# Kernel optimization log

Measured on AMD Instinct MI355X. Metric: run time of the kernel, lower is better.

Reference implementation:

```python
import jax, jax.numpy as jnp
import numpy as np

EPS = 1e-5  # torch BatchNorm1d default eps
N, E, F, H, P = 50000, 640000, 128, 128, 64


def batch_norm(h):
    # track_running_stats=False, affine=False -> per-batch mean / biased var
    mu = jnp.mean(h, axis=0)
    var = jnp.mean((h - mu) ** 2, axis=0)
    return (h - mu) * jax.lax.rsqrt(var + EPS)


def gcn_conv(x, src, dst, W, b, n_nodes):
    # GCNConv: D^{-1/2} (A + I) D^{-1/2} X W + b
    h = x @ W
    loop = jnp.arange(n_nodes)
    s = jnp.concatenate([src, loop])
    d = jnp.concatenate([dst, loop])
    deg = jax.ops.segment_sum(jnp.ones(s.shape[0], h.dtype), d, num_segments=n_nodes)
    inv_sqrt = jax.lax.rsqrt(jnp.maximum(deg, 1.0))  # deg >= 1 due to self loops
    msg = h[s] * (inv_sqrt[s] * inv_sqrt[d])[:, None]  # [E+N, H]
    return jax.ops.segment_sum(msg, d, num_segments=n_nodes) + b


def setup_inputs() -> dict:
    key = jax.random.key(0)
    ks = jax.random.split(key, 12)
    s = 0.05
    return {
        "x": jax.random.normal(ks[0], (N, F), jnp.float32),
        "core_values": jax.random.uniform(ks[1], (N,), jnp.float32),
        "W0": jax.random.normal(ks[2], (F, H), jnp.float32) * s,
        "b0": jnp.zeros((H,), jnp.float32),
        "W1": jax.random.normal(ks[3], (H, H), jnp.float32) * s,
        "b1": jnp.zeros((H,), jnp.float32),
        "lin1_W": jax.random.normal(ks[4], (3 * H, H), jnp.float32) * s,
        "lin1_b": jnp.zeros((H,), jnp.float32),
        "lin2_W": jax.random.normal(ks[5], (H, 1), jnp.float32) * s,
        "lin2_b": jnp.zeros((1,), jnp.float32),
        "edge_index": jax.random.randint(ks[6], (2, E), 0, N, jnp.int64 if jax.config.read("jax_enable_x64") else jnp.int32),
        "part_id": jax.random.randint(ks[7], (N,), 0, P, jnp.int32),
        "curr_node_id": 123,
        "num_partitions": P,
    }


def reference(x, core_values, W0, b0, W1, b1, lin1_W, lin1_b, lin2_W, lin2_b,
              edge_index, part_id, curr_node_id, num_partitions):
    n_nodes = x.shape[0]
    src, dst = edge_index[0], edge_index[1]

    # GNN stack: conv -> batchnorm -> relu (num_layers = 2)
    for W, b in ((W0, b0), (W1, b1)):
        x = jax.nn.relu(batch_norm(gcn_conv(x, src, dst, W, b, n_nodes)))

    # getPartitonEmbedding_usingCoreValue as fused segment reductions
    cv = core_values[:, None]
    core = jax.ops.segment_sum(x * cv, part_id, num_segments=num_partitions)
    non_core = jax.ops.segment_sum(x * (1.0 - cv), part_id, num_segments=num_partitions)
    partition_embedding = jnp.concatenate([core, non_core], axis=1)  # [P, 2H]

    x_curr = jnp.broadcast_to(x[curr_node_id][None, :], (num_partitions, x.shape[1]))
    z = jnp.concatenate([x_curr, partition_embedding], axis=1)  # [P, 3H]
    z = jax.nn.relu(z @ lin1_W + lin1_b)
    return z @ lin2_W + lin2_b  # [P, 1]
```

## Files before the change

kernel.cpp:

```cpp
#include <hip/hip_runtime.h>
#include <math.h>

#define EPSV 1e-5f
#define PSORT_NB 256
#define SCAN_NB 256

typedef __attribute__((ext_vector_type(8))) short bf16x8;
typedef __attribute__((ext_vector_type(4))) float f32x4;

__device__ __forceinline__ uint f2b(float f) {
  uint u = __builtin_bit_cast(uint, f);
  return (u + 0x7FFFu + ((u >> 16) & 1u)) >> 16;
}
__device__ __forceinline__ float blo(uint v) { return __builtin_bit_cast(float, v << 16); }
__device__ __forceinline__ float bhi(uint v) { return __builtin_bit_cast(float, v & 0xFFFF0000u); }
__device__ __forceinline__ float b2f(ushort u) { return __builtin_bit_cast(float, ((uint)u) << 16); }

__global__ __launch_bounds__(256) void k_pre1(int* __restrict__ hist, int nbZero,
                                              const int* __restrict__ part,
                                              int* __restrict__ blockHist,
                                              const float* __restrict__ W0,
                                              const float* __restrict__ W1,
                                              ushort* __restrict__ WT0,
                                              ushort* __restrict__ WT1, int n) {
  const int b = blockIdx.x, tid = threadIdx.x;
  if (b < nbZero) {
    int i = b * 256 + tid;
    if (i < n) hist[i] = 0;
  } else if (b < nbZero + PSORT_NB) {
    __shared__ int lh[64];
    int pb = b - nbZero;
    if (tid < 64) lh[tid] = 0;
    __syncthreads();
    int chunk = (n + PSORT_NB - 1) / PSORT_NB;
    int beg = pb * chunk, end = min(n, beg + chunk);
    for (int i = beg + tid; i < end; i += 256) atomicAdd(&lh[part[i]], 1);
    __syncthreads();
    if (tid < 64) blockHist[pb * 64 + tid] = lh[tid];
  } else {
    int idx = (b - nbZero - PSORT_NB) * 256 + tid;
    const float* W = (idx < 16384) ? W0 : W1;
    ushort* WT = (idx < 16384) ? WT0 : WT1;
    int j = idx & 16383;
    int c = j >> 7, k = j & 127;
    WT[j] = (ushort)f2b(W[k * 128 + c]);
  }
}

__global__ __launch_bounds__(256) void k_pre2(const int* __restrict__ dst,
                                              int* __restrict__ hist,
                                              int* __restrict__ rank, int e, int eb,
                                              const int* __restrict__ blockHist,
                                              int* __restrict__ base,
                                              int* __restrict__ ptot) {
  const int b = blockIdx.x, tid = threadIdx.x;
  if (b < eb) {
    int i = b * 256 + tid;
    if (i < e) rank[i] = atomicAdd(&hist[dst[i]], 1);
  } else {
    __shared__ int wtot[4];
    const int p = b - eb;
    const int lane = tid & 63, w = tid >> 6;
    int v = blockHist[tid * 64 + p];
    int x = v;
    #pragma unroll
    for (int off = 1; off < 64; off <<= 1) {
      int y = __shfl_up(x, off);
      if (lane >= off) x += y;
    }
    if (lane == 63) wtot[w] = x;
    __syncthreads();
    int woff = 0;
    if (w > 0) woff = wtot[0];
    if (w > 1) woff += wtot[1];
    if (w > 2) woff += wtot[2];
    base[tid * 64 + p] = woff + x - v;
    if (tid == 255) ptot[p] = woff + x;
  }
}

__global__ __launch_bounds__(256) void k_pre3(const int* __restrict__ hist,
                                              int* __restrict__ row_start,
                                              float* __restrict__ invs,
                                              int* __restrict__ bsum, int n,
                                              const int* __restrict__ ptot,
                                              int* __restrict__ pexcl,
                                              int* __restrict__ pstart) {
  const int b = blockIdx.x, tid = threadIdx.x;
  if (b < SCAN_NB) {
    __shared__ int wtot[4];
    __shared__ int tot;
    const int lane = tid & 63, w = tid >> 6;
    const int chunk = (n + SCAN_NB - 1) / SCAN_NB;
    const int beg = b * chunk, end = min(n, beg + chunk);
    int running = 0;
    for (int t0 = beg; t0 < end; t0 += 256) {
      int i = t0 + tid;
      int v = (i < end) ? hist[i] : 0;
      int x = v;
      #pragma unroll
      for (int off = 1; off < 64; off <<= 1) {
        int y = __shfl_up(x, off);
        if (lane >= off) x += y;
      }
      if (lane == 63) wtot[w] = x;
      __syncthreads();
      if (tid == 0) {
        int a0 = wtot[0], a1 = wtot[1], a2 = wtot[2], a3 = wtot[3];
        wtot[0] = 0; wtot[1] = a0; wtot[2] = a0 + a1; wtot[3] = a0 + a1 + a2;
        tot = a0 + a1 + a2 + a3;
      }
      __syncthreads();
      if (i < end) {
        row_start[i] = running + wtot[w] + x - v;
        invs[i] = rsqrtf((float)(v + 1));
      }
      running += tot;
      __syncthreads();
    }
    if (tid == 0) bsum[b] = running;
  } else if (tid < 64) {
    int v = ptot[tid];
    int x = v;
    #pragma unroll
    for (int off = 1; off < 64; off <<= 1) {
      int y = __shfl_up(x, off);
      if (tid >= off) x += y;
    }
    int excl = x - v;
    pexcl[tid] = excl;
    pstart[tid] = excl;
    if (tid == 63) pstart[64] = x;
  }
}

__global__ __launch_bounds__(256) void k_pre4(const int* __restrict__ bsum,
                                              int* __restrict__ boff,
                                              int* __restrict__ row_fin, int n,
                                              const int* __restrict__ part,
                                              const int* __restrict__ base,
                                              const int* __restrict__ pexcl,
                                              int* __restrict__ perm) {
  const int b = blockIdx.x, tid = threadIdx.x;
  if (b == 0) {
    if (tid < 64) {
      int v0 = bsum[tid * 4], v1 = bsum[tid * 4 + 1], v2 = bsum[tid * 4 + 2], v3 = bsum[tid * 4 + 3];
      int s = v0 + v1 + v2 + v3;
      int x = s;
      #pragma unroll
      for (int off = 1; off < 64; off <<= 1) {
        int y = __shfl_up(x, off);
        if (tid >= off) x += y;
      }
      int run = x - s;
      boff[tid * 4] = run; run += v0;
      boff[tid * 4 + 1] = run; run += v1;
      boff[tid * 4 + 2] = run; run += v2;
      boff[tid * 4 + 3] = run;
      if (tid == 63) row_fin[n] = x;
    }
  } else {
    __shared__ int cur[64];
    const int pb = b - 1;
    if (tid < 64) cur[tid] = base[pb * 64 + tid] + pexcl[tid];
    __syncthreads();
    int chunk = (n + PSORT_NB - 1) / PSORT_NB;
    int beg = pb * chunk, end = min(n, beg + chunk);
    for (int i = beg + tid; i < end; i += 256) {
      int pos = atomicAdd(&cur[part[i]], 1);
      perm[pos] = i;
    }
  }
}

template <bool BN>
__device__ __forceinline__ void gemm_body(ushort* As, ushort* Bs, float* muL, float* sclL,
                                          const void* __restrict__ inp,
                                          const ushort* __restrict__ WT,
                                          const float* __restrict__ invs,
                                          const float* __restrict__ stats_red,
                                          ushort* __restrict__ outb, int n, int bb) {
  const int tid = threadIdx.x;
  const int l = tid & 63, w = tid >> 6;
  const int br0 = bb * 128;

  if (BN) {
    if (tid < 128) {
      float s = stats_red[tid], q = stats_red[128 + tid];
      float m = s * (1.0f / 50000.0f);
      muL[tid] = m;
      sclL[tid] = rsqrtf(q * (1.0f / 50000.0f) - m * m + EPSV);
    }
    __syncthreads();
  }

  #pragma unroll
  for (int i = 0; i < 8; ++i) {
    int flat = i * 2048 + tid * 8;
    int c = flat >> 7;
    uint4 v = *(const uint4*)&WT[flat];
    *(uint4*)&Bs[flat ^ ((c & 7) << 3)] = v;
  }
  #pragma unroll
  for (int i = 0; i < 8; ++i) {
    int flat = i * 2048 + tid * 8;
    int row = flat >> 7, k0 = flat & 127;
    int grow = br0 + row;
    uint4 u;
    if (grow < n) {
      if (BN) {
        const ushort* inb = (const ushort*)inp;
        uint4 raw = *(const uint4*)&inb[(size_t)grow * 128 + k0];
        float f[8] = {blo(raw.x), bhi(raw.x), blo(raw.y), bhi(raw.y),
                      blo(raw.z), bhi(raw.z), blo(raw.w), bhi(raw.w)};
        #pragma unroll
        for (int j = 0; j < 8; ++j) {
          float v = (f[j] - muL[k0 + j]) * sclL[k0 + j];
          f[j] = v > 0.f ? v : 0.f;
        }
        u.x = f2b(f[0]) | (f2b(f[1]) << 16);
        u.y = f2b(f[2]) | (f2b(f[3]) << 16);
        u.z = f2b(f[4]) | (f2b(f[5]) << 16);
        u.w = f2b(f[6]) | (f2b(f[7]) << 16);
      } else {
        const float* inf = (const float*)inp;
        float4 v0 = *(const float4*)&inf[(size_t)grow * 128 + k0];
        float4 v1 = *(const float4*)&inf[(size_t)grow * 128 + k0 + 4];
        u.x = f2b(v0.x) | (f2b(v0.y) << 16);
        u.y = f2b(v0.z) | (f2b(v0.w) << 16);
        u.z = f2b(v1.x) | (f2b(v1.y) << 16);
        u.w = f2b(v1.z) | (f2b(v1.w) << 16);
      }
    } else {
      u.x = u.y = u.z = u.w = 0u;
    }
    *(uint4*)&As[flat ^ ((row & 7) << 3)] = u;
  }
  __syncthreads();

  const int wr = w >> 1, wc = w & 1;
  const int lr = l & 15, lk = (l >> 4) * 8;
  f32x4 acc[4][4];
  #pragma unroll
  for (int m = 0; m < 4; ++m)
    #pragma unroll
    for (int nn = 0; nn < 4; ++nn) acc[m][nn] = (f32x4){0.f, 0.f, 0.f, 0.f};

  #pragma unroll
  for (int ks = 0; ks < 4; ++ks) {
    bf16x8 af[4], bfr[4];
    #pragma unroll
    for (int m = 0; m < 4; ++m) {
      int row = wr * 64 + m * 16 + lr;
      af[m] = *(const bf16x8*)&As[(row * 128 + ks * 32 + lk) ^ ((row & 7) << 3)];
    }
    #pragma unroll
    for (int nn = 0; nn < 4; ++nn) {
      int c = wc * 64 + nn * 16 + lr;
      bfr[nn] = *(const bf16x8*)&Bs[(c * 128 + ks * 32 + lk) ^ ((c & 7) << 3)];
    }
    #pragma unroll
    for (int m = 0; m < 4; ++m)
      #pragma unroll
      for (int nn = 0; nn < 4; ++nn)
        acc[m][nn] = __builtin_amdgcn_mfma_f32_16x16x32_bf16(af[m], bfr[nn], acc[m][nn], 0, 0, 0);
  }

  #pragma unroll
  for (int m = 0; m < 4; ++m) {
    #pragma unroll
    for (int r = 0; r < 4; ++r) {
      int row = br0 + wr * 64 + m * 16 + (l >> 4) * 4 + r;
      if (row >= n) continue;
      float iv = invs[row];
      #pragma unroll
      for (int nn = 0; nn < 4; ++nn) {
        int col = wc * 64 + nn * 16 + lr;
        outb[(size_t)row * 128 + col] = (ushort)f2b(acc[m][nn][r] * iv);
      }
    }
  }
}

__global__ __launch_bounds__(256) void k_mega1(const float* __restrict__ x,
                                               const ushort* __restrict__ WT0,
                                               const float* __restrict__ invs,
                                               ushort* __restrict__ hsb, int n, int gb,
                                               const int* __restrict__ row_start,
                                               const int* __restrict__ boff,
                                               int* __restrict__ row_fin,
                                               const int* __restrict__ src,
                                               const int* __restrict__ dst,
                                               const int* __restrict__ rank,
                                               int* __restrict__ csr, int e) {
  __shared__ ushort As[16384];
  __shared__ ushort Bs[16384];
  const int b = blockIdx.x, tid = threadIdx.x;
  if (b < gb) {
    gemm_body<false>(As, Bs, nullptr, nullptr, x, WT0, invs, nullptr, hsb, n, b);
  } else if (b < gb + SCAN_NB) {
    const int sb = b - gb;
    const int chunk = (n + SCAN_NB - 1) / SCAN_NB;
    const int beg = sb * chunk, end = min(n, beg + chunk);
    const int off = boff[sb];
    for (int i = beg + tid; i < end; i += 256) row_fin[i] = row_start[i] + off;
  } else {
    const int chunkS = (n + SCAN_NB - 1) / SCAN_NB;
    int i = (b - gb - SCAN_NB) * 256 + tid;
    if (i < e) {
      int d = dst[i];
      csr[row_start[d] + boff[d / chunkS] + rank[i]] = src[i];
    }
  }
}

template <bool BN>
__global__ __launch_bounds__(256) void k_gemm(const void* __restrict__ inp,
                                              const ushort* __restrict__ WT,
                                              const float* __restrict__ invs,
                                              const float* __restrict__ stats_red,
                                              ushort* __restrict__ outb, int n) {
  __shared__ ushort As[16384];
  __shared__ ushort Bs[16384];
  __shared__ float muL[128], sclL[128];
  gemm_body<BN>(As, Bs, muL, sclL, inp, WT, invs, stats_red, outb, n, blockIdx.x);
}

__global__ __launch_bounds__(256) void k_gather(const ushort* __restrict__ hsb,
                                                const int* __restrict__ row_fin,
                                                const int* __restrict__ csr,
                                                const float* __restrict__ invs,
                                                const float* __restrict__ bias,
                                                ushort* __restrict__ outb,
                                                float* __restrict__ statsP, int n) {
  const int tid = threadIdx.x;
  const int lane = tid & 63, w = tid >> 6;
  const int c0 = lane * 2;
  const ushort* hc = hsb + c0;
  float s0 = 0.f, s1 = 0.f, q0 = 0.f, q1 = 0.f;
  const float bv0 = bias[c0], bv1 = bias[c0 + 1];
  const int stride = gridDim.x * 4;
  for (int node = blockIdx.x * 4 + w; node < n; node += stride) {
    uint vs = *(const uint*)&hc[(size_t)node * 128];
    float accx = blo(vs), accy = bhi(vs);
    int beg = row_fin[node], end = row_fin[node + 1];
    int deg = end - beg;
    int base = 0;
    while (base < deg) {
      int cnt = min(deg - base, 64);
      int sidx = 0;
      if (lane < cnt) sidx = csr[beg + base + lane];
      int j = 0;
      for (; j + 7 < cnt; j += 8) {
        int sA = __shfl(sidx, j + 0), sB = __shfl(sidx, j + 1);
        int sC = __shfl(sidx, j + 2), sD = __shfl(sidx, j + 3);
        int sE = __shfl(sidx, j + 4), sF = __shfl(sidx, j + 5);
        int sG = __shfl(sidx, j + 6), sH = __shfl(sidx, j + 7);
        uint vA = *(const uint*)&hc[(size_t)sA * 128];
        uint vB = *(const uint*)&hc[(size_t)sB * 128];
        uint vC = *(const uint*)&hc[(size_t)sC * 128];
        uint vD = *(const uint*)&hc[(size_t)sD * 128];
        uint vE = *(const uint*)&hc[(size_t)sE * 128];
        uint vF = *(const uint*)&hc[(size_t)sF * 128];
        uint vG = *(const uint*)&hc[(size_t)sG * 128];
        uint vH = *(const uint*)&hc[(size_t)sH * 128];
        accx += ((blo(vA) + blo(vB)) + (blo(vC) + blo(vD))) +
                ((blo(vE) + blo(vF)) + (blo(vG) + blo(vH)));
        accy += ((bhi(vA) + bhi(vB)) + (bhi(vC) + bhi(vD))) +
                ((bhi(vE) + bhi(vF)) + (bhi(vG) + bhi(vH)));
      }
      for (; j + 3 < cnt; j += 4) {
        int sA = __shfl(sidx, j + 0), sB = __shfl(sidx, j + 1);
        int sC = __shfl(sidx, j + 2), sD = __shfl(sidx, j + 3);
        uint vA = *(const uint*)&hc[(size_t)sA * 128];
        uint vB = *(const uint*)&hc[(size_t)sB * 128];
        uint vC = *(const uint*)&hc[(size_t)sC * 128];
        uint vD = *(const uint*)&hc[(size_t)sD * 128];
        accx += (blo(vA) + blo(vB)) + (blo(vC) + blo(vD));
        accy += (bhi(vA) + bhi(vB)) + (bhi(vC) + bhi(vD));
      }
      for (; j < cnt; ++j) {
        int sA = __shfl(sidx, j);
        uint vA = *(const uint*)&hc[(size_t)sA * 128];
        accx += blo(vA);
        accy += bhi(vA);
      }
      base += cnt;
    }
    float iv = invs[node];
    float o0 = accx * iv + bv0, o1 = accy * iv + bv1;
    *(uint*)&outb[(size_t)node * 128 + c0] = f2b(o0) | (f2b(o1) << 16);
    s0 += o0; s1 += o1; q0 += o0 * o0; q1 += o1 * o1;
  }
  __shared__ float redS[4][128], redQ[4][128];
  redS[w][c0] = s0; redS[w][c0 + 1] = s1;
  redQ[w][c0] = q0; redQ[w][c0 + 1] = q1;
  __syncthreads();
  if (tid < 128) {
    float s = redS[0][tid] + redS[1][tid] + redS[2][tid] + redS[3][tid];
    statsP[blockIdx.x * 256 + tid] = s;
  } else {
    int t = tid - 128;
    float q = redQ[0][t] + redQ[1][t] + redQ[2][t] + redQ[3][t];
    statsP[blockIdx.x * 256 + tid] = q;
  }
}

__global__ __launch_bounds__(1024) void k_finstats(const float* __restrict__ statsP,
                                                   float* __restrict__ stats_red,
                                                   int nb) {
  int t = threadIdx.x;
  int c = blockIdx.x * 16 + (t & 15);
  int b0 = t >> 4;
  int per = nb >> 6;
  float s = 0.f;
  for (int j = 0; j < per; ++j) s += statsP[(b0 * per + j) * 256 + c];
  __shared__ float red[1024];
  red[t] = s;
  __syncthreads();
  for (int st = 512; st >= 16; st >>= 1) {
    if (t < st) red[t] += red[t + st];
    __syncthreads();
  }
  if (t < 16) stats_red[blockIdx.x * 16 + t] = red[t];
}

__global__ __launch_bounds__(512) void k_pool2(const ushort* __restrict__ hb,
                                               const float* __restrict__ stats_red,
                                               const float* __restrict__ cv,
                                               const int* __restrict__ perm,
                                               const int* __restrict__ pstart,
                                               float* __restrict__ poolP, int n) {
  const int tid = threadIdx.x;
  const int lane = tid & 63, w = tid >> 6;
  const int p = blockIdx.x >> 2, s = blockIdx.x & 3;
  const int g = s * 8 + w;
  const int c0 = lane * 2;

  float s0 = stats_red[c0], s1 = stats_red[c0 + 1];
  float qq0 = stats_red[128 + c0], qq1 = stats_red[128 + c0 + 1];
  float mu0 = s0 * (1.0f / 50000.0f), mu1 = s1 * (1.0f / 50000.0f);
  float scl0 = rsqrtf(qq0 * (1.0f / 50000.0f) - mu0 * mu0 + EPSV);
  float scl1 = rsqrtf(qq1 * (1.0f / 50000.0f) - mu1 * mu1 + EPSV);

  const int beg = pstart[p], end = pstart[p + 1];
  float cc0 = 0.f, cc1 = 0.f, cn0 = 0.f, cn1 = 0.f;

  int j = beg + g;
  for (; j + 32 < end; j += 64) {
    int rA = perm[j], rB = perm[j + 32];
    uint vA = *(const uint*)&hb[(size_t)rA * 128 + c0];
    uint vB = *(const uint*)&hb[(size_t)rB * 128 + c0];
    float cvA = cv[rA], cvB = cv[rB];
    float xA0 = (blo(vA) - mu0) * scl0; xA0 = xA0 > 0.f ? xA0 : 0.f;
    float xA1 = (bhi(vA) - mu1) * scl1; xA1 = xA1 > 0.f ? xA1 : 0.f;
    float xB0 = (blo(vB) - mu0) * scl0; xB0 = xB0 > 0.f ? xB0 : 0.f;
    float xB1 = (bhi(vB) - mu1) * scl1; xB1 = xB1 > 0.f ? xB1 : 0.f;
    cc0 += xA0 * cvA + xB0 * cvB;
    cc1 += xA1 * cvA + xB1 * cvB;
    cn0 += xA0 * (1.f - cvA) + xB0 * (1.f - cvB);
    cn1 += xA1 * (1.f - cvA) + xB1 * (1.f - cvB);
  }
  if (j < end) {
    int rA = perm[j];
    uint vA = *(const uint*)&hb[(size_t)rA * 128 + c0];
    float cvA = cv[rA];
    float xA0 = (blo(vA) - mu0) * scl0; xA0 = xA0 > 0.f ? xA0 : 0.f;
    float xA1 = (bhi(vA) - mu1) * scl1; xA1 = xA1 > 0.f ? xA1 : 0.f;
    cc0 += xA0 * cvA;
    cc1 += xA1 * cvA;
    cn0 += xA0 * (1.f - cvA);
    cn1 += xA1 * (1.f - cvA);
  }

  __shared__ float redC[8][128], redN[8][128];
  redC[w][c0] = cc0; redC[w][c0 + 1] = cc1;
  redN[w][c0] = cn0; redN[w][c0 + 1] = cn1;
  __syncthreads();
  if (tid < 128) {
    float a = 0.f;
    #pragma unroll
    for (int ww = 0; ww < 8; ++ww) a += redC[ww][tid];
    poolP[blockIdx.x * 256 + tid] = a;
  } else if (tid < 256) {
    int t = tid - 128;
    float a = 0.f;
    #pragma unroll
    for (int ww = 0; ww < 8; ++ww) a += redN[ww][t];
    poolP[blockIdx.x * 256 + tid] = a;
  }
}

__global__ __launch_bounds__(128) void k_mlp(const ushort* __restrict__ hb,
                                             const float* __restrict__ stats_red,
                                             const float* __restrict__ poolP,
                                             const float* __restrict__ l1W,
                                             const float* __restrict__ l1b,
                                             const float* __restrict__ l2W,
                                             const float* __restrict__ l2b,
                                             const int* __restrict__ curr_ptr,
                                             float* __restrict__ out, int n) {
  const int p = blockIdx.x;
  const int t = threadIdx.x;
  __shared__ float z[384];
  int curr = *curr_ptr;
  float s = stats_red[t], q = stats_red[128 + t];
  float mu = s / (float)n;
  float scl = rsqrtf(q / (float)n - mu * mu + EPSV);
  float v = b2f(hb[(size_t)curr * 128 + t]);
  v = (v - mu) * scl;
  z[t] = v > 0.f ? v : 0.f;
  float ccore = 0.f, cnon = 0.f;
  #pragma unroll
  for (int sb = 0; sb < 4; ++sb) {
    ccore += poolP[(p * 4 + sb) * 256 + t];
    cnon  += poolP[(p * 4 + sb) * 256 + 128 + t];
  }
  z[128 + t] = ccore;
  z[256 + t] = cnon;
  __syncthreads();
  float a = l1b[t];
  for (int k = 0; k < 384; ++k) a += z[k] * l1W[k * 128 + t];
  a = a > 0.f ? a : 0.f;
  float pr = a * l2W[t];
  #pragma unroll
  for (int off = 32; off; off >>= 1) pr += __shfl_down(pr, off);
  __shared__ float rr[2];
  if ((t & 63) == 0) rr[t >> 6] = pr;
  __syncthreads();
  if (t == 0) out[p] = rr[0] + rr[1] + l2b[0];
}

extern "C" void kernel_launch(void* const* d_in, const int* in_sizes, int n_in,
                              void* d_out, int out_size, void* d_ws, size_t ws_size,
                              hipStream_t stream) {
  const float* x    = (const float*)d_in[0];
  const float* cv   = (const float*)d_in[1];
  const float* W0   = (const float*)d_in[2];
  const float* b0   = (const float*)d_in[3];
  const float* W1   = (const float*)d_in[4];
  const float* b1   = (const float*)d_in[5];
  const float* l1W  = (const float*)d_in[6];
  const float* l1b  = (const float*)d_in[7];
  const float* l2W  = (const float*)d_in[8];
  const float* l2b  = (const float*)d_in[9];
  const int*   ei   = (const int*)d_in[10];
  const int*   part = (const int*)d_in[11];
  const int*   curr = (const int*)d_in[12];

  const int N = in_sizes[1];
  const int E = in_sizes[10] / 2;
  const int* src = ei;
  const int* dst = ei + E;

  const int GATHER_BLOCKS = 2048;

  char* w = (char*)d_ws;
  size_t off = 0;
  auto alloc = [&](size_t bytes) -> void* {
    void* p = (void*)(w + off);
    off = (off + bytes + 255) & ~(size_t)255;
    return p;
  };
  int*   hist      = (int*)alloc((size_t)N * 4);
  int*   row_start = (int*)alloc((size_t)(N + 1) * 4);
  int*   row_fin   = (int*)alloc((size_t)(N + 1) * 4);
  int*   csr       = (int*)alloc((size_t)E * 4);
  int*   rank      = (int*)alloc((size_t)E * 4);
  float* invs      = (float*)alloc((size_t)N * 4);
  int*   bsum      = (int*)alloc((size_t)SCAN_NB * 4);
  int*   boff      = (int*)alloc((size_t)SCAN_NB * 4);
  int*   blockHist = (int*)alloc((size_t)PSORT_NB * 64 * 4);
  int*   pbase     = (int*)alloc((size_t)PSORT_NB * 64 * 4);
  int*   ptot      = (int*)alloc(64 * 4);
  int*   pexcl     = (int*)alloc(64 * 4);
  int*   pstart    = (int*)alloc(65 * 4);
  int*   perm      = (int*)alloc((size_t)N * 4);
  float* stats_red0 = (float*)alloc(256 * 4);
  float* stats_red1 = (float*)alloc(256 * 4);
  float* statsP    = (float*)alloc((size_t)GATHER_BLOCKS * 256 * 4);
  float* poolP     = (float*)alloc((size_t)256 * 256 * 4);
  ushort* WT0      = (ushort*)alloc((size_t)16384 * 2);
  ushort* WT1      = (ushort*)alloc((size_t)16384 * 2);
  ushort* hsb      = (ushort*)alloc((size_t)N * 128 * 2);
  ushort* hb       = (ushort*)alloc((size_t)N * 128 * 2);
  (void)ws_size;

  const int eb = (E + 255) / 256;
  const int nbZero = (N + 255) / 256;
  const int gb = (N + 127) / 128;

  k_pre1<<<nbZero + PSORT_NB + 128, 256, 0, stream>>>(hist, nbZero, part, blockHist,
                                                      W0, W1, WT0, WT1, N);
  k_pre2<<<eb + 64, 256, 0, stream>>>(dst, hist, rank, E, eb, blockHist, pbase, ptot);
  k_pre3<<<SCAN_NB + 1, 256, 0, stream>>>(hist, row_start, invs, bsum, N, ptot, pexcl, pstart);
  k_pre4<<<1 + PSORT_NB, 256, 0, stream>>>(bsum, boff, row_fin, N, part, pbase, pexcl, perm);
  k_mega1<<<gb + SCAN_NB + eb, 256, 0, stream>>>(x, WT0, invs, hsb, N, gb,
                                                 row_start, boff, row_fin,
                                                 src, dst, rank, csr, E);
  k_gather<<<GATHER_BLOCKS, 256, 0, stream>>>(hsb, row_fin, csr, invs, b0, hb, statsP, N);
  k_finstats<<<16, 1024, 0, stream>>>(statsP, stats_red0, GATHER_BLOCKS);
  k_gemm<true><<<gb, 256, 0, stream>>>(hb, WT1, invs, stats_red0, hsb, N);
  k_gather<<<GATHER_BLOCKS, 256, 0, stream>>>(hsb, row_fin, csr, invs, b1, hb, statsP, N);
  k_finstats<<<16, 1024, 0, stream>>>(statsP, stats_red1, GATHER_BLOCKS);
  k_pool2<<<256, 512, 0, stream>>>(hb, stats_red1, cv, perm, pstart, poolP, N);
  k_mlp<<<64, 128, 0, stream>>>(hb, stats_red1, poolP, l1W, l1b, l2W, l2b, curr, (float*)d_out, N);
}
```

Baseline: 176.5 us.

## Move first GEMM earlier by deferring degree scaling into gather

The first-layer GEMM no longer depends on the degree normalization, so it is launched together with the edge-rank atomics and partition scan in one kernel, right after the first preprocessing kernel. The source-side inverse-sqrt-degree scaling for layer one moves into the gather, which now loads invs per neighbor and shuffles it alongside the indices. The CSR fill becomes its own kernel. This overlaps the GEMM with the atomic histogram work. In exchange the first gather does extra per-edge loads and multiplies, and the 4-wide unrolled remainder loop is removed.

```diff
diff --git a/kernel.cpp b/kernel.cpp
--- a/kernel.cpp
+++ b/kernel.cpp
@@ -47,133 +47,7 @@
   }
 }
 
-__global__ __launch_bounds__(256) void k_pre2(const int* __restrict__ dst,
-                                              int* __restrict__ hist,
-                                              int* __restrict__ rank, int e, int eb,
-                                              const int* __restrict__ blockHist,
-                                              int* __restrict__ base,
-                                              int* __restrict__ ptot) {
-  const int b = blockIdx.x, tid = threadIdx.x;
-  if (b < eb) {
-    int i = b * 256 + tid;
-    if (i < e) rank[i] = atomicAdd(&hist[dst[i]], 1);
-  } else {
-    __shared__ int wtot[4];
-    const int p = b - eb;
-    const int lane = tid & 63, w = tid >> 6;
-    int v = blockHist[tid * 64 + p];
-    int x = v;
-    #pragma unroll
-    for (int off = 1; off < 64; off <<= 1) {
-      int y = __shfl_up(x, off);
-      if (lane >= off) x += y;
-    }
-    if (lane == 63) wtot[w] = x;
-    __syncthreads();
-    int woff = 0;
-    if (w > 0) woff = wtot[0];
-    if (w > 1) woff += wtot[1];
-    if (w > 2) woff += wtot[2];
-    base[tid * 64 + p] = woff + x - v;
-    if (tid == 255) ptot[p] = woff + x;
-  }
-}
-
-__global__ __launch_bounds__(256) void k_pre3(const int* __restrict__ hist,
-                                              int* __restrict__ row_start,
-                                              float* __restrict__ invs,
-                                              int* __restrict__ bsum, int n,
-                                              const int* __restrict__ ptot,
-                                              int* __restrict__ pexcl,
-                                              int* __restrict__ pstart) {
-  const int b = blockIdx.x, tid = threadIdx.x;
-  if (b < SCAN_NB) {
-    __shared__ int wtot[4];
-    __shared__ int tot;
-    const int lane = tid & 63, w = tid >> 6;
-    const int chunk = (n + SCAN_NB - 1) / SCAN_NB;
-    const int beg = b * chunk, end = min(n, beg + chunk);
-    int running = 0;
-    for (int t0 = beg; t0 < end; t0 += 256) {
-      int i = t0 + tid;
-      int v = (i < end) ? hist[i] : 0;
-      int x = v;
-      #pragma unroll
-      for (int off = 1; off < 64; off <<= 1) {
-        int y = __shfl_up(x, off);
-        if (lane >= off) x += y;
-      }
-      if (lane == 63) wtot[w] = x;
-      __syncthreads();
-      if (tid == 0) {
-        int a0 = wtot[0], a1 = wtot[1], a2 = wtot[2], a3 = wtot[3];
-        wtot[0] = 0; wtot[1] = a0; wtot[2] = a0 + a1; wtot[3] = a0 + a1 + a2;
-        tot = a0 + a1 + a2 + a3;
-      }
-      __syncthreads();
-      if (i < end) {
-        row_start[i] = running + wtot[w] + x - v;
-        invs[i] = rsqrtf((float)(v + 1));
-      }
-      running += tot;
-      __syncthreads();
-    }
-    if (tid == 0) bsum[b] = running;
-  } else if (tid < 64) {
-    int v = ptot[tid];
-    int x = v;
-    #pragma unroll
-    for (int off = 1; off < 64; off <<= 1) {
-      int y = __shfl_up(x, off);
-      if (tid >= off) x += y;
-    }
-    int excl = x - v;
-    pexcl[tid] = excl;
-    pstart[tid] = excl;
-    if (tid == 63) pstart[64] = x;
-  }
-}
-
-__global__ __launch_bounds__(256) void k_pre4(const int* __restrict__ bsum,
-                                              int* __restrict__ boff,
-                                              int* __restrict__ row_fin, int n,
-                                              const int* __restrict__ part,
-                                              const int* __restrict__ base,
-                                              const int* __restrict__ pexcl,
-                                              int* __restrict__ perm) {
-  const int b = blockIdx.x, tid = threadIdx.x;
-  if (b == 0) {
-    if (tid < 64) {
-      int v0 = bsum[tid * 4], v1 = bsum[tid * 4 + 1], v2 = bsum[tid * 4 + 2], v3 = bsum[tid * 4 + 3];
-      int s = v0 + v1 + v2 + v3;
-      int x = s;
-      #pragma unroll
-      for (int off = 1; off < 64; off <<= 1) {
-        int y = __shfl_up(x, off);
-        if (tid >= off) x += y;
-      }
-      int run = x - s;
-      boff[tid * 4] = run; run += v0;
-      boff[tid * 4 + 1] = run; run += v1;
-      boff[tid * 4 + 2] = run; run += v2;
-      boff[tid * 4 + 3] = run;
-      if (tid == 63) row_fin[n] = x;
-    }
-  } else {
-    __shared__ int cur[64];
-    const int pb = b - 1;
-    if (tid < 64) cur[tid] = base[pb * 64 + tid] + pexcl[tid];
-    __syncthreads();
-    int chunk = (n + PSORT_NB - 1) / PSORT_NB;
-    int beg = pb * chunk, end = min(n, beg + chunk);
-    for (int i = beg + tid; i < end; i += 256) {
-      int pos = atomicAdd(&cur[part[i]], 1);
-      perm[pos] = i;
-    }
-  }
-}
-
-template <bool BN>
+template <bool BN, bool INV>
 __device__ __forceinline__ void gemm_body(ushort* As, ushort* Bs, float* muL, float* sclL,
                                           const void* __restrict__ inp,
                                           const ushort* __restrict__ WT,
@@ -272,60 +146,185 @@
     for (int r = 0; r < 4; ++r) {
       int row = br0 + wr * 64 + m * 16 + (l >> 4) * 4 + r;
       if (row >= n) continue;
-      float iv = invs[row];
+      float iv = INV ? invs[row] : 1.0f;
       #pragma unroll
       for (int nn = 0; nn < 4; ++nn) {
         int col = wc * 64 + nn * 16 + lr;
-        outb[(size_t)row * 128 + col] = (ushort)f2b(acc[m][nn][r] * iv);
-      }
-    }
-  }
-}
-
-__global__ __launch_bounds__(256) void k_mega1(const float* __restrict__ x,
+        float v = acc[m][nn][r];
+        if (INV) v *= iv;
+        outb[(size_t)row * 128 + col] = (ushort)f2b(v);
+      }
+    }
+  }
+}
+
+__global__ __launch_bounds__(256) void k_mega2(const float* __restrict__ x,
                                                const ushort* __restrict__ WT0,
-                                               const float* __restrict__ invs,
                                                ushort* __restrict__ hsb, int n, int gb,
-                                               const int* __restrict__ row_start,
+                                               const int* __restrict__ dst,
+                                               int* __restrict__ hist,
+                                               int* __restrict__ rank, int e, int eb,
+                                               const int* __restrict__ blockHist,
+                                               int* __restrict__ base,
+                                               int* __restrict__ ptot) {
+  __shared__ ushort As[16384];
+  __shared__ ushort Bs[16384];
+  const int b = blockIdx.x, tid = threadIdx.x;
+  if (b < gb) {
+    gemm_body<false, false>(As, Bs, nullptr, nullptr, x, WT0, nullptr, nullptr, hsb, n, b);
+  } else if (b < gb + eb) {
+    int i = (b - gb) * 256 + tid;
+    if (i < e) rank[i] = atomicAdd(&hist[dst[i]], 1);
+  } else {
+    __shared__ int wtot[4];
+    const int p = b - gb - eb;
+    const int lane = tid & 63, w = tid >> 6;
+    int v = blockHist[tid * 64 + p];
+    int x2 = v;
+    #pragma unroll
+    for (int off = 1; off < 64; off <<= 1) {
+      int y = __shfl_up(x2, off);
+      if (lane >= off) x2 += y;
+    }
+    if (lane == 63) wtot[w] = x2;
+    __syncthreads();
+    int woff = 0;
+    if (w > 0) woff = wtot[0];
+    if (w > 1) woff += wtot[1];
+    if (w > 2) woff += wtot[2];
+    base[tid * 64 + p] = woff + x2 - v;
+    if (tid == 255) ptot[p] = woff + x2;
+  }
+}
+
+__global__ __launch_bounds__(256) void k_pre3(const int* __restrict__ hist,
+                                              int* __restrict__ row_start,
+                                              float* __restrict__ invs,
+                                              int* __restrict__ bsum, int n,
+                                              const int* __restrict__ ptot,
+                                              int* __restrict__ pexcl,
+                                              int* __restrict__ pstart) {
+  const int b = blockIdx.x, tid = threadIdx.x;
+  if (b < SCAN_NB) {
+    __shared__ int wtot[4];
+    __shared__ int tot;
+    const int lane = tid & 63, w = tid >> 6;
+    const int chunk = (n + SCAN_NB - 1) / SCAN_NB;
+    const int beg = b * chunk, end = min(n, beg + chunk);
+    int running = 0;
+    for (int t0 = beg; t0 < end; t0 += 256) {
+      int i = t0 + tid;
+      int v = (i < end) ? hist[i] : 0;
+      int x = v;
+      #pragma unroll
+      for (int off = 1; off < 64; off <<= 1) {
+        int y = __shfl_up(x, off);
+        if (lane >= off) x += y;
+      }
+      if (lane == 63) wtot[w] = x;
+      __syncthreads();
+      if (tid == 0) {
+        int a0 = wtot[0], a1 = wtot[1], a2 = wtot[2], a3 = wtot[3];
+        wtot[0] = 0; wtot[1] = a0; wtot[2] = a0 + a1; wtot[3] = a0 + a1 + a2;
+        tot = a0 + a1 + a2 + a3;
+      }
+      __syncthreads();
+      if (i < end) {
+        row_start[i] = running + wtot[w] + x - v;
+        invs[i] = rsqrtf((float)(v + 1));
+      }
+      running += tot;
+      __syncthreads();
+    }
+    if (tid == 0) bsum[b] = running;
+  } else if (tid < 64) {
+    int v = ptot[tid];
+    int x = v;
+    #pragma unroll
+    for (int off = 1; off < 64; off <<= 1) {
+      int y = __shfl_up(x, off);
+      if (tid >= off) x += y;
+    }
+    int excl = x - v;
+    pexcl[tid] = excl;
+    pstart[tid] = excl;
+    if (tid == 63) pstart[64] = x;
+  }
+}
+
+__global__ __launch_bounds__(256) void k_pre4(const int* __restrict__ bsum,
+                                              int* __restrict__ boff,
+                                              int* __restrict__ row_fin, int n,
+                                              const int* __restrict__ part,
+                                              const int* __restrict__ base,
+                                              const int* __restrict__ pexcl,
+                                              int* __restrict__ perm) {
+  const int b = blockIdx.x, tid = threadIdx.x;
+  if (b == 0) {
+    if (tid < 64) {
+      int v0 = bsum[tid * 4], v1 = bsum[tid * 4 + 1], v2 = bsum[tid * 4 + 2], v3 = bsum[tid * 4 + 3];
+      int s = v0 + v1 + v2 + v3;
+      int x = s;
+      #pragma unroll
+      for (int off = 1; off < 64; off <<= 1) {
+        int y = __shfl_up(x, off);
+        if (tid >= off) x += y;
+      }
+      int run = x - s;
+      boff[tid * 4] = run; run += v0;
+      boff[tid * 4 + 1] = run; run += v1;
+      boff[tid * 4 + 2] = run; run += v2;
+      boff[tid * 4 + 3] = run;
+      if (tid == 63) row_fin[n] = x;
+    }
+  } else {
+    __shared__ int cur[64];
+    const int pb = b - 1;
+    if (tid < 64) cur[tid] = base[pb * 64 + tid] + pexcl[tid];
+    __syncthreads();
+    int chunk = (n + PSORT_NB - 1) / PSORT_NB;
+    int beg = pb * chunk, end = min(n, beg + chunk);
+    for (int i = beg + tid; i < end; i += 256) {
+      int pos = atomicAdd(&cur[part[i]], 1);
+      perm[pos] = i;
+    }
+  }
+}
+
+__global__ __launch_bounds__(256) void k_mega5(const int* __restrict__ row_start,
                                                const int* __restrict__ boff,
-                                               int* __restrict__ row_fin,
+                                               int* __restrict__ row_fin, int n,
                                                const int* __restrict__ src,
                                                const int* __restrict__ dst,
                                                const int* __restrict__ rank,
                                                int* __restrict__ csr, int e) {
-  __shared__ ushort As[16384];
-  __shared__ ushort Bs[16384];
   const int b = blockIdx.x, tid = threadIdx.x;
-  if (b < gb) {
-    gemm_body<false>(As, Bs, nullptr, nullptr, x, WT0, invs, nullptr, hsb, n, b);
-  } else if (b < gb + SCAN_NB) {
-    const int sb = b - gb;
-    const int chunk = (n + SCAN_NB - 1) / SCAN_NB;
-    const int beg = sb * chunk, end = min(n, beg + chunk);
-    const int off = boff[sb];
+  const int chunk = (n + SCAN_NB - 1) / SCAN_NB;
+  if (b < SCAN_NB) {
+    const int beg = b * chunk, end = min(n, beg + chunk);
+    const int off = boff[b];
     for (int i = beg + tid; i < end; i += 256) row_fin[i] = row_start[i] + off;
   } else {
-    const int chunkS = (n + SCAN_NB - 1) / SCAN_NB;
-    int i = (b - gb - SCAN_NB) * 256 + tid;
+    int i = (b - SCAN_NB) * 256 + tid;
     if (i < e) {
       int d = dst[i];
-      csr[row_start[d] + boff[d / chunkS] + rank[i]] = src[i];
-    }
-  }
-}
-
-template <bool BN>
-__global__ __launch_bounds__(256) void k_gemm(const void* __restrict__ inp,
-                                              const ushort* __restrict__ WT,
-                                              const float* __restrict__ invs,
-                                              const float* __restrict__ stats_red,
-                                              ushort* __restrict__ outb, int n) {
+      csr[row_start[d] + boff[d / chunk] + rank[i]] = src[i];
+    }
+  }
+}
+
+__global__ __launch_bounds__(256) void k_gemm2(const ushort* __restrict__ inp,
+                                               const ushort* __restrict__ WT,
+                                               const float* __restrict__ invs,
+                                               const float* __restrict__ stats_red,
+                                               ushort* __restrict__ outb, int n) {
   __shared__ ushort As[16384];
   __shared__ ushort Bs[16384];
   __shared__ float muL[128], sclL[128];
-  gemm_body<BN>(As, Bs, muL, sclL, inp, WT, invs, stats_red, outb, n, blockIdx.x);
-}
-
+  gemm_body<true, true>(As, Bs, muL, sclL, inp, WT, invs, stats_red, outb, n, blockIdx.x);
+}
+
+template <bool EINV>
 __global__ __launch_bounds__(256) void k_gather(const ushort* __restrict__ hsb,
                                                 const int* __restrict__ row_fin,
                                                 const int* __restrict__ csr,
@@ -342,14 +341,21 @@
   const int stride = gridDim.x * 4;
   for (int node = blockIdx.x * 4 + w; node < n; node += stride) {
     uint vs = *(const uint*)&hc[(size_t)node * 128];
-    float accx = blo(vs), accy = bhi(vs);
+    float iv_d = invs[node];
+    float accx, accy;
+    if (EINV) { accx = iv_d * blo(vs); accy = iv_d * bhi(vs); }
+    else      { accx = blo(vs);        accy = bhi(vs); }
     int beg = row_fin[node], end = row_fin[node + 1];
     int deg = end - beg;
     int base = 0;
     while (base < deg) {
       int cnt = min(deg - base, 64);
       int sidx = 0;
-      if (lane < cnt) sidx = csr[beg + base + lane];
+      float siv = 0.f;
+      if (lane < cnt) {
+        sidx = csr[beg + base + lane];
+        if (EINV) siv = invs[sidx];
+      }
       int j = 0;
       for (; j + 7 < cnt; j += 8) {
         int sA = __shfl(sidx, j + 0), sB = __shfl(sidx, j + 1);
@@ -364,31 +370,37 @@
         uint vF = *(const uint*)&hc[(size_t)sF * 128];
         uint vG = *(const uint*)&hc[(size_t)sG * 128];
         uint vH = *(const uint*)&hc[(size_t)sH * 128];
-        accx += ((blo(vA) + blo(vB)) + (blo(vC) + blo(vD))) +
-                ((blo(vE) + blo(vF)) + (blo(vG) + blo(vH)));
-        accy += ((bhi(vA) + bhi(vB)) + (bhi(vC) + bhi(vD))) +
-                ((bhi(vE) + bhi(vF)) + (bhi(vG) + bhi(vH)));
-      }
-      for (; j + 3 < cnt; j += 4) {
-        int sA = __shfl(sidx, j + 0), sB = __shfl(sidx, j + 1);
-        int sC = __shfl(sidx, j + 2), sD = __shfl(sidx, j + 3);
-        uint vA = *(const uint*)&hc[(size_t)sA * 128];
-        uint vB = *(const uint*)&hc[(size_t)sB * 128];
-        uint vC = *(const uint*)&hc[(size_t)sC * 128];
-        uint vD = *(const uint*)&hc[(size_t)sD * 128];
-        accx += (blo(vA) + blo(vB)) + (blo(vC) + blo(vD));
-        accy += (bhi(vA) + bhi(vB)) + (bhi(vC) + bhi(vD));
+        if (EINV) {
+          float fA = __shfl(siv, j + 0), fB = __shfl(siv, j + 1);
+          float fC = __shfl(siv, j + 2), fD = __shfl(siv, j + 3);
+          float fE = __shfl(siv, j + 4), fF = __shfl(siv, j + 5);
+          float fG = __shfl(siv, j + 6), fH = __shfl(siv, j + 7);
+          accx += fA * blo(vA) + fB * blo(vB) + fC * blo(vC) + fD * blo(vD) +
+                  fE * blo(vE) + fF * blo(vF) + fG * blo(vG) + fH * blo(vH);
+          accy += fA * bhi(vA) + fB * bhi(vB) + fC * bhi(vC) + fD * bhi(vD) +
+                  fE * bhi(vE) + fF * bhi(vF) + fG * bhi(vG) + fH * bhi(vH);
+        } else {
+          accx += ((blo(vA) + blo(vB)) + (blo(vC) + blo(vD))) +
+                  ((blo(vE) + blo(vF)) + (blo(vG) + blo(vH)));
+          accy += ((bhi(vA) + bhi(vB)) + (bhi(vC) + bhi(vD))) +
+                  ((bhi(vE) + bhi(vF)) + (bhi(vG) + bhi(vH)));
+        }
       }
       for (; j < cnt; ++j) {
         int sA = __shfl(sidx, j);
         uint vA = *(const uint*)&hc[(size_t)sA * 128];
-        accx += blo(vA);
-        accy += bhi(vA);
+        if (EINV) {
+          float fA = __shfl(siv, j);
+          accx += fA * blo(vA);
+          accy += fA * bhi(vA);
+        } else {
+          accx += blo(vA);
+          accy += bhi(vA);
+        }
       }
       base += cnt;
     }
-    float iv = invs[node];
-    float o0 = accx * iv + bv0, o1 = accy * iv + bv1;
+    float o0 = accx * iv_d + bv0, o1 = accy * iv_d + bv1;
     *(uint*)&outb[(size_t)node * 128 + c0] = f2b(o0) | (f2b(o1) << 16);
     s0 += o0; s1 += o1; q0 += o0 * o0; q1 += o1 * o1;
   }
@@ -592,16 +604,16 @@
 
   k_pre1<<<nbZero + PSORT_NB + 128, 256, 0, stream>>>(hist, nbZero, part, blockHist,
                                                       W0, W1, WT0, WT1, N);
-  k_pre2<<<eb + 64, 256, 0, stream>>>(dst, hist, rank, E, eb, blockHist, pbase, ptot);
+  k_mega2<<<gb + eb + 64, 256, 0, stream>>>(x, WT0, hsb, N, gb,
+                                            dst, hist, rank, E, eb,
+                                            blockHist, pbase, ptot);
   k_pre3<<<SCAN_NB + 1, 256, 0, stream>>>(hist, row_start, invs, bsum, N, ptot, pexcl, pstart);
   k_pre4<<<1 + PSORT_NB, 256, 0, stream>>>(bsum, boff, row_fin, N, part, pbase, pexcl, perm);
-  k_mega1<<<gb + SCAN_NB + eb, 256, 0, stream>>>(x, WT0, invs, hsb, N, gb,
-                                                 row_start, boff, row_fin,
-                                                 src, dst, rank, csr, E);
-  k_gather<<<GATHER_BLOCKS, 256, 0, stream>>>(hsb, row_fin, csr, invs, b0, hb, statsP, N);
+  k_mega5<<<SCAN_NB + eb, 256, 0, stream>>>(row_start, boff, row_fin, N, src, dst, rank, csr, E);
+  k_gather<true><<<GATHER_BLOCKS, 256, 0, stream>>>(hsb, row_fin, csr, invs, b0, hb, statsP, N);
   k_finstats<<<16, 1024, 0, stream>>>(statsP, stats_red0, GATHER_BLOCKS);
-  k_gemm<true><<<gb, 256, 0, stream>>>(hb, WT1, invs, stats_red0, hsb, N);
-  k_gather<<<GATHER_BLOCKS, 256, 0, stream>>>(hsb, row_fin, csr, invs, b1, hb, statsP, N);
+  k_gemm2<<<gb, 256, 0, stream>>>(hb, WT1, invs, stats_red0, hsb, N);
+  k_gather<false><<<GATHER_BLOCKS, 256, 0, stream>>>(hsb, row_fin, csr, invs, b1, hb, statsP, N);
   k_finstats<<<16, 1024, 0, stream>>>(statsP, stats_red1, GATHER_BLOCKS);
   k_pool2<<<256, 512, 0, stream>>>(hb, stats_red1, cv, perm, pstart, poolP, N);
   k_mlp<<<64, 128, 0, stream>>>(hb, stats_red1, poolP, l1W, l1b, l2W, l2b, curr, (float*)d_out, N);
```

Measured after the change: 175.1 us. Within noise of the previous version (-0.8%).
